# Kernel optimization log

Measured on AMD Instinct MI355X. Metric: run time of the kernel, lower is better.

The kernel has to match this reference:

```python
import jax, jax.numpy as jnp
import numpy as np

BETA = 0.25
ENTROPY_LOSS_RATIO = 0.1
TEMPERATURE = 0.01
EPS = 1e-5


def _l2norm(x):
    return x / jnp.sqrt(jnp.sum(x * x, axis=-1, keepdims=True)).clip(1e-12)


def _entropy_loss(affinity):
    # affinity: [N, n_e]
    a = affinity / TEMPERATURE
    probs = jax.nn.softmax(a, axis=-1)
    log_probs = jax.nn.log_softmax(a + EPS, axis=-1)
    avg_probs = jnp.mean(probs, axis=0)
    avg_entropy = -jnp.sum(avg_probs * jnp.log(avg_probs + EPS))
    sample_entropy = -jnp.mean(jnp.sum(probs * log_probs, axis=-1))
    return sample_entropy - avg_entropy


def setup_inputs() -> dict:
    key = jax.random.key(0)
    k1, k2, k3 = jax.random.split(key, 3)
    B, C, H, W = 16, 256, 32, 32
    n_e = 16384
    z = jax.random.normal(k1, (B, C, H, W), dtype=jnp.float32)
    embedding = jax.random.normal(k2, (n_e, C), dtype=jnp.float32) * 0.02
    query_ids = jax.random.randint(k3, (B, 1), 0, W, dtype=jnp.int64)
    return {"z": z, "embedding": embedding, "query_ids": query_ids}


def reference(z, embedding, query_ids):
    B, C, H, W = z.shape
    sg = jax.lax.stop_gradient
    zt = jnp.transpose(z, (0, 2, 3, 1))            # [B,H,W,C]
    # l2_norm=True path
    zt = _l2norm(zt)
    emb = _l2norm(embedding)                       # [n_e, C]
    zf = zt.reshape(-1, C)                         # [N, C]
    d = (jnp.sum(zf * zf, axis=1, keepdims=True)
         + jnp.sum(emb * emb, axis=1)
         - 2.0 * jnp.einsum('nd,kd->nk', zf, emb))  # [N, n_e]
    idx = jnp.argmin(d, axis=1)                    # [N]
    z_q = emb[idx].reshape(zt.shape)               # [B,H,W,C]

    # dead code rate (unbiased std over batch, per token position)
    code = idx.reshape(B, -1).astype(jnp.float32)
    dead_code_rate = jnp.mean((jnp.std(code, axis=0, ddof=1) < 1e-5).astype(jnp.float32))

    vq_loss = jnp.mean((z_q - sg(zt)) ** 2, axis=-1, keepdims=True)      # [B,H,W,1]
    commit_loss = BETA * jnp.mean((sg(z_q) - zt) ** 2, axis=-1, keepdims=True)
    loss_mask = (jnp.arange(W).reshape(1, 1, -1, 1)
                 <= query_ids[:, -1].reshape(-1, 1, 1, 1)).astype(jnp.float32)
    denom = jnp.sum(loss_mask)
    vq_loss = jnp.sum(vq_loss * loss_mask) / denom
    commit_loss = jnp.sum(commit_loss * loss_mask) / denom
    entropy_loss = ENTROPY_LOSS_RATIO * _entropy_loss(-d)

    # straight-through estimator
    z_q_st = zt + sg(z_q - zt)
    z_q_out = jnp.transpose(z_q_st, (0, 3, 1, 2))  # [B,C,H,W]
    return (z_q_out, vq_loss, commit_loss, entropy_loss, dead_code_rate, idx)
```

## Files before the change

kernel.cpp:

```cpp
#include <hip/hip_runtime.h>
#include <math.h>

#define N_TOK   16384
#define N_E     16384
#define CDIM    256
#define NCH     8
#define CHSZ    (N_E / NCH)
#define L2E100  144.26950408889634f
#define DELTA_C 0.06f
#define DELTA_D 0.03f
#define EPS_NT  0.008f
#define CAP_BLK 1536u
#define NT_CAP  65536u

typedef __attribute__((ext_vector_type(8))) short short8;
typedef __attribute__((ext_vector_type(4))) float f32x4;

#define OFF_A2   0u
#define OFF_B2   2097152u
#define OFF_RMX  4194304u
#define OFF_CS   4210688u
#define OFF_SC   4227072u
#define OFF_RK   4227088u
#define OFF_NT   4259856u
#define OFF_NTC  4325392u
#define OFF_CBC  4325408u
#define OFF_IDX  4327456u
#define OFF_CAND 4343840u
#define OFF_ZT   10635296u
#define NEED_ZT_BYTES 59318400ull

__device__ __forceinline__ unsigned short f2bf(float x) {
  unsigned u = __float_as_uint(x);
  unsigned r = (u + 0x7fffu + ((u >> 16) & 1u)) >> 16;
  return (unsigned short)r;
}
__device__ __forceinline__ float bf2f(unsigned short h) {
  return __uint_as_float(((unsigned)h) << 16);
}
__device__ __forceinline__ unsigned fkey(float f) {
  unsigned u = __float_as_uint(f);
  return (u & 0x80000000u) ? ~u : (u | 0x80000000u);
}
__device__ __forceinline__ float keyf(unsigned k) {
  return (k & 0x80000000u) ? __uint_as_float(k ^ 0x80000000u) : __uint_as_float(~k);
}

__device__ __forceinline__ void async_load16(const void* g, void* l) {
  __builtin_amdgcn_global_load_lds((const __attribute__((address_space(1))) void*)g,
                                   (__attribute__((address_space(3))) void*)l, 16, 0, 0);
}

__device__ __forceinline__ float blockReduceSum256(float v, float* sbuf) {
  __syncthreads();
  v += __shfl_down(v, 32);
  v += __shfl_down(v, 16);
  v += __shfl_down(v, 8);
  v += __shfl_down(v, 4);
  v += __shfl_down(v, 2);
  v += __shfl_down(v, 1);
  const int tid = threadIdx.x;
  if ((tid & 63) == 0) sbuf[tid >> 6] = v;
  __syncthreads();
  return sbuf[0] + sbuf[1] + sbuf[2] + sbuf[3];
}

__global__ __launch_bounds__(256) void k_norm_emb(const float* __restrict__ emb,
    unsigned short* __restrict__ B2, float* __restrict__ colsum,
    float* __restrict__ scalars, unsigned long long* __restrict__ rowkey,
    unsigned* __restrict__ ntc, unsigned* __restrict__ rowMaxU) {
  const int tid = threadIdx.x, lane = tid & 63, wv = tid >> 6;
  if (blockIdx.x < 64) {
    const int i = blockIdx.x * 256 + tid;
    colsum[i] = 0.f;
    rowkey[i] = ~0ull;
    rowMaxU[i] = 0u;
    if (i < 16) { scalars[i] = 0.f; ntc[i] = 0u; }
  }
  const int k = blockIdx.x * 4 + wv;
  const float4 v = *(const float4*)&emb[(size_t)k * CDIM + lane * 4];
  float ss = v.x * v.x + v.y * v.y + v.z * v.z + v.w * v.w;
#pragma unroll
  for (int off = 1; off < 64; off <<= 1) ss += __shfl_xor(ss, off);
  const float r = 1.0f / fmaxf(sqrtf(ss), 1e-12f);
  ushort4 o;
  o.x = f2bf(v.x * r); o.y = f2bf(v.y * r);
  o.z = f2bf(v.z * r); o.w = f2bf(v.w * r);
  *(ushort4*)&B2[(size_t)k * CDIM + lane * 4] = o;
}

__global__ __launch_bounds__(256) void k_norm_z(const float* __restrict__ z,
                                                unsigned short* __restrict__ A2,
                                                float* __restrict__ zT) {
  __shared__ float ssb[4][64];
  __shared__ float rn[64];
  __shared__ unsigned short tile[64 * 264];
  __shared__ float tileF[64 * 260];
  const int b = blockIdx.x >> 4, hw0 = (blockIdx.x & 15) * 64;
  const int tid = threadIdx.x, cg = tid >> 6, hwl = tid & 63;
  float ss = 0.f;
#pragma unroll 8
  for (int i = 0; i < 64; ++i) {
    const int c = cg + i * 4;
    const float x = z[((size_t)(b * CDIM + c) << 10) + hw0 + hwl];
    ss = fmaf(x, x, ss);
  }
  ssb[cg][hwl] = ss;
  __syncthreads();
  if (tid < 64) {
    const float t = ssb[0][tid] + ssb[1][tid] + ssb[2][tid] + ssb[3][tid];
    rn[tid] = 1.0f / fmaxf(sqrtf(t), 1e-12f);
  }
  __syncthreads();
  const float r = rn[hwl];
#pragma unroll 8
  for (int i = 0; i < 64; ++i) {
    const int c = cg + i * 4;
    const float x = z[((size_t)(b * CDIM + c) << 10) + hw0 + hwl];
    tile[hwl * 264 + c] = f2bf(x * r);
    tileF[hwl * 260 + c] = x;
  }
  __syncthreads();
  const int rr = tid >> 5, tt = tid & 31;
#pragma unroll
  for (int it = 0; it < 8; ++it) {
    const int row = rr + 8 * it;
    const int token = b * 1024 + hw0 + row;
    const uint4 v = *(const uint4*)&tile[row * 264 + tt * 8];
    *(uint4*)&A2[(size_t)token * CDIM + tt * 8] = v;
    if (zT != nullptr) {
      const float4 f0 = *(const float4*)&tileF[row * 260 + tt * 4];
      const float4 f1 = *(const float4*)&tileF[row * 260 + 128 + tt * 4];
      *(float4*)&zT[(size_t)token * CDIM + tt * 4] = f0;
      *(float4*)&zT[(size_t)token * CDIM + 128 + tt * 4] = f1;
    }
  }
}

__global__ __launch_bounds__(256, 3) void k_pass1(const unsigned short* __restrict__ A2,
    const unsigned short* __restrict__ B2,
    unsigned long long* __restrict__ cand, unsigned* __restrict__ cbc,
    unsigned* __restrict__ rowMaxU) {
  __shared__ alignas(16) unsigned short Bt[2][128 * 64];
  __shared__ unsigned lcnt;
  const int rt = blockIdx.x, chunk = blockIdx.y;
  const int r0 = rt * 64, k0 = chunk * CHSZ;
  const int blin = rt * NCH + chunk;
  const int tid = threadIdx.x, lane = tid & 63, w = tid >> 6;
  const int wr0 = w * 16;
  const int l15 = lane & 15, quad = lane >> 4;

  if (tid == 0) lcnt = 0u;

  short8 afr[4][2];
  {
    const size_t rbase = (size_t)(r0 + wr0 + l15) * CDIM;
#pragma unroll
    for (int st = 0; st < 4; ++st)
#pragma unroll
      for (int kk = 0; kk < 2; ++kk)
        afr[st][kk] = *(const short8*)&A2[rbase + st * 64 + (((kk << 2) | quad) * 8)];
  }

  const int row0 = tid >> 3, cg0 = tid & 7;
  const int gcg0 = cg0 ^ (row0 & 7);
  const unsigned short* bsrc0 = B2 + (size_t)(k0 + row0) * CDIM + gcg0 * 8;
  const unsigned bofs0 = (unsigned)tid * 16u;

  int boff[8][2];
#pragma unroll
  for (int tj = 0; tj < 8; ++tj) {
    const int br = tj * 16 + l15;
#pragma unroll
    for (int kk = 0; kk < 2; ++kk)
      boff[tj][kk] = br * 64 + ((((kk << 2) | quad) ^ (br & 7)) * 8);
  }

#pragma unroll
  for (int i = 0; i < 4; ++i)
    async_load16(bsrc0 + i * 8192, (char*)Bt[0] + bofs0 + i * 4096);
  __syncthreads();

  f32x4 acc[8];
  float runMax[4];
#pragma unroll
  for (int r = 0; r < 4; ++r) runMax[r] = -3.0e38f;

#pragma unroll 1
  for (int ct = 0; ct < 16; ++ct) {
#pragma unroll
    for (int tj = 0; tj < 8; ++tj) acc[tj] = (f32x4){0.f, 0.f, 0.f, 0.f};

#pragma unroll
    for (int st = 0; st < 4; ++st) {
      if (!(ct == 15 && st == 3)) {
        const int noff = (st < 3) ? (st + 1) * 64 : 32768;
        char* dbuf = (char*)Bt[(st + 1) & 1];
#pragma unroll
        for (int i = 0; i < 4; ++i)
          async_load16(bsrc0 + noff + i * 8192, dbuf + bofs0 + i * 4096);
      }
      const unsigned short* bp = Bt[st & 1];
#pragma unroll
      for (int kk = 0; kk < 2; ++kk) {
        short8 bfr[8];
#pragma unroll
        for (int tj = 0; tj < 8; ++tj)
          bfr[tj] = *(const short8*)&bp[boff[tj][kk]];
#pragma unroll
        for (int tj = 0; tj < 8; ++tj)
          acc[tj] = __builtin_amdgcn_mfma_f32_16x16x32_bf16(afr[st][kk], bfr[tj],
                                                            acc[tj], 0, 0, 0);
      }

      if (st == 3) {
        const int kb = k0 + ct * 128;
#pragma unroll
        for (int r = 0; r < 4; ++r) {
          float mt = acc[0][r];
#pragma unroll
          for (int tj = 1; tj < 8; ++tj) mt = fmaxf(mt, acc[tj][r]);
          mt = fmaxf(mt, __shfl_xor(mt, 1));
          mt = fmaxf(mt, __shfl_xor(mt, 2));
          mt = fmaxf(mt, __shfl_xor(mt, 4));
          mt = fmaxf(mt, __shfl_xor(mt, 8));
          runMax[r] = fmaxf(runMax[r], mt);
          const float thrD = runMax[r] - DELTA_D;
          const unsigned rowg = (unsigned)(r0 + wr0 + quad * 4 + r);
#pragma unroll
          for (int tj = 0; tj < 8; ++tj) {
            const float d = acc[tj][r];
            if (d >= thrD) {
              const unsigned slot = atomicAdd(&lcnt, 1u);
              if (slot < CAP_BLK) {
                const float t = d + d;
                const unsigned pr = (rowg << 14) | (unsigned)(kb + tj * 16 + l15);
                cand[(size_t)blin * CAP_BLK + slot] =
                    ((unsigned long long)__float_as_uint(t) << 32) | pr;
              }
            }
          }
        }
      }
      __syncthreads();
    }
    bsrc0 += 32768;
  }

#pragma unroll
  for (int r = 0; r < 4; ++r)
    if (l15 == 0)
      atomicMax(&rowMaxU[r0 + wr0 + quad * 4 + r], fkey(runMax[r] + runMax[r]));
  if (tid == 0) cbc[blin] = lcnt < CAP_BLK ? lcnt : CAP_BLK;
}

__global__ __launch_bounds__(256) void k_cstat2(const unsigned long long* __restrict__ cand,
    const unsigned* __restrict__ cbc, const unsigned* __restrict__ rowMaxU,
    float* __restrict__ colsum, unsigned* __restrict__ ntList,
    unsigned* __restrict__ ntc, float* __restrict__ scalars) {
  __shared__ float lM[64], lZ[64], lE[64], lIZ[64];
  __shared__ float sbuf[4];
  const int rt = blockIdx.x, r0 = rt * 64;
  const int tid = threadIdx.x, lane = tid & 63;
  if (tid < 64) {
    lM[tid] = keyf(rowMaxU[r0 + tid]);
    lZ[tid] = 0.f; lE[tid] = 0.f;
  }
  __syncthreads();
  for (int sub = 0; sub < NCH; ++sub) {
    const int blin = rt * NCH + sub;
    const unsigned cnt = cbc[blin] < CAP_BLK ? cbc[blin] : CAP_BLK;
    for (unsigned i = tid; i < cnt; i += 256u) {
      const unsigned long long e = cand[(size_t)blin * CAP_BLK + i];
      const unsigned pr = (unsigned)(e & 0xFFFFFFFu);
      const float t = __uint_as_float((unsigned)(e >> 32));
      const int rowl = (int)((pr >> 14) & 63u);
      const float d = t - lM[rowl];
      const float ex = exp2f(d * L2E100);
      atomicAdd(&lZ[rowl], ex);
      atomicAdd(&lE[rowl], d * 100.0f * ex);
    }
  }
  __syncthreads();
  float ent = 0.f;
  if (tid < 64) {
    const float Z = lZ[tid];
    lIZ[tid] = 1.0f / Z;
    ent = logf(Z) - lE[tid] / Z;
  }
  const float es = blockReduceSum256(ent, sbuf);
  if (tid == 0) atomicAdd(&scalars[1], es);
  __syncthreads();
  for (int sub = 0; sub < NCH; ++sub) {
    const int blin = rt * NCH + sub;
    const unsigned cnt = cbc[blin] < CAP_BLK ? cbc[blin] : CAP_BLK;
    const unsigned lim = (cnt + 255u) & ~255u;
    for (unsigned i = tid; i < lim; i += 256u) {
      bool nt = false;
      unsigned pr = 0u;
      if (i < cnt) {
        const unsigned long long e = cand[(size_t)blin * CAP_BLK + i];
        pr = (unsigned)(e & 0xFFFFFFFu);
        const float t = __uint_as_float((unsigned)(e >> 32));
        const int rowl = (int)((pr >> 14) & 63u);
        const float d = t - lM[rowl];
        atomicAdd(&colsum[pr & 0x3FFFu], exp2f(d * L2E100) * lIZ[rowl]);
        nt = (d >= -EPS_NT);
      }
      const unsigned long long mask = __ballot(nt);
      const unsigned cw = (unsigned)__popcll(mask);
      unsigned base = 0u;
      if (lane == 0 && cw) base = atomicAdd(ntc, cw);
      base = __shfl((int)base, 0);
      if (nt) {
        const unsigned off = (unsigned)__popcll(mask & ((1ull << lane) - 1ull));
        const unsigned s = base + off;
        if (s < NT_CAP) ntList[s] = pr;
      }
    }
  }
}

__global__ __launch_bounds__(256) void k_refine(const float* __restrict__ z,
    const float* __restrict__ zT, const float* __restrict__ emb,
    const unsigned* __restrict__ ntList, const unsigned* __restrict__ ntc,
    unsigned long long* __restrict__ rowkey) {
  const unsigned cnt = *ntc;
  const unsigned lim = cnt < NT_CAP ? cnt : NT_CAP;
  const int lane = threadIdx.x & 63, wv = threadIdx.x >> 6;
  for (unsigned slot = blockIdx.x * 4 + wv; slot < lim; slot += gridDim.x * 4) {
    const unsigned pr = ntList[slot];
    const int n = (int)(pr >> 14), k = (int)(pr & 0x3FFFu);
    const int b = n >> 10, hw = n & 1023;
    double sz = 0.0, se = 0.0, sp = 0.0;
#pragma unroll
    for (int u = 0; u < CDIM / 64; ++u) {
      const int c = lane + u * 64;
      const double zv = (zT != nullptr)
          ? (double)zT[(size_t)n * CDIM + c]
          : (double)z[((size_t)(b * CDIM + c) << 10) + hw];
      const double ev = (double)emb[(size_t)k * CDIM + c];
      sz = fma(zv, zv, sz); se = fma(ev, ev, se); sp = fma(zv, ev, sp);
    }
    for (int off = 32; off; off >>= 1) {
      sz += __shfl_down(sz, off);
      se += __shfl_down(se, off);
      sp += __shfl_down(sp, off);
    }
    if (lane == 0) {
      const double nz = fmax(sqrt(sz), 1e-12);
      const double ne = fmax(sqrt(se), 1e-12);
      const double d = sz / (nz * nz) + se / (ne * ne) - 2.0 * sp / (nz * ne);
      const unsigned long long key =
          (((unsigned long long)(d * 140737488355328.0)) << 14) | (unsigned long long)k;
      atomicMin(&rowkey[n], key);
    }
  }
}

__global__ __launch_bounds__(256) void k_zq(const unsigned short* __restrict__ A2,
    const unsigned short* __restrict__ B2, const unsigned long long* __restrict__ rowkey,
    const long long* __restrict__ qids, int* __restrict__ idxI,
    float* __restrict__ outIdxF, float* __restrict__ outZ,
    float* __restrict__ scalars) {
  __shared__ int lidx[64];
  __shared__ unsigned short tile[64 * 264];
  __shared__ float sbuf[4];
  const int b = blockIdx.x >> 4, hw0 = (blockIdx.x & 15) * 64;
  const int tid = threadIdx.x;
  if (tid < 64) {
    const int n = b * 1024 + hw0 + tid;
    const unsigned long long key = rowkey[n];
    const int k = (key != ~0ull) ? (int)(key & 0x3FFFull) : 0;
    lidx[tid] = k;
    idxI[n] = k;
    outIdxF[n] = (float)k;
  }
  __syncthreads();
  const long long qid = qids[b];
  const int rr = tid >> 5, tt = tid & 31;
  float vq = 0.f;
#pragma unroll
  for (int it = 0; it < 8; ++it) {
    const int row = rr + 8 * it;
    const int token = b * 1024 + hw0 + row;
    union { uint4 v; unsigned short s[8]; } ev, zv;
    ev.v = *(const uint4*)&B2[(size_t)lidx[row] * CDIM + tt * 8];
    zv.v = *(const uint4*)&A2[(size_t)token * CDIM + tt * 8];
    *(uint4*)&tile[row * 264 + tt * 8] = ev.v;
    float dd = 0.f;
#pragma unroll
    for (int u = 0; u < 8; ++u) {
      const float d = bf2f(ev.s[u]) - bf2f(zv.s[u]);
      dd = fmaf(d, d, dd);
    }
    if ((long long)(row & 31) <= qid) vq += dd;
  }
  const float s = blockReduceSum256(vq, sbuf);
  if (tid == 0) atomicAdd(&scalars[0], s * (1.0f / 256.0f));
  __syncthreads();
  const int cg = tid >> 6, hwl = tid & 63;
#pragma unroll 8
  for (int i = 0; i < 64; ++i) {
    const int c = cg + i * 4;
    outZ[((size_t)(b * CDIM + c) << 10) + hw0 + hwl] = bf2f(tile[hwl * 264 + c]);
  }
}

__global__ __launch_bounds__(256) void k_final(const int* __restrict__ idxI,
    const long long* __restrict__ qids, const float* __restrict__ colsum,
    const float* __restrict__ scalars, float* __restrict__ out) {
  __shared__ float sbuf[4];
  const int tid = threadIdx.x;
  float ae = 0.f;
  for (int i = tid; i < N_E; i += 256) {
    const float q = colsum[i] * (1.0f / (float)N_TOK);
    ae += q * logf(q + 1e-5f);
  }
  const float aes = blockReduceSum256(ae, sbuf);
  int cnt = 0;
  for (int p = tid; p < 1024; p += 256) {
    const int v = idxI[p];
    bool eq = true;
    for (int b = 1; b < 16; ++b) eq = eq && (idxI[b * 1024 + p] == v);
    cnt += eq ? 1 : 0;
  }
  const float dc = blockReduceSum256((float)cnt, sbuf);
  if (tid == 0) {
    float denom = 0.f;
    for (int b = 0; b < 16; ++b) denom += (float)(qids[b] + 1ll);
    out[4194304] = scalars[0] / denom;
    out[4194305] = 0.25f * scalars[0] / denom;
    out[4194306] = 0.1f * (scalars[1] * (1.0f / (float)N_TOK) + aes);
    out[4194307] = dc * (1.0f / 1024.0f);
  }
}

extern "C" void kernel_launch(void* const* d_in, const int* in_sizes, int n_in,
                              void* d_out, int out_size, void* d_ws, size_t ws_size,
                              hipStream_t stream) {
  const float*      z    = (const float*)d_in[0];
  const float*      emb  = (const float*)d_in[1];
  const long long*  qids = (const long long*)d_in[2];
  float* out = (float*)d_out;
  float* W   = (float*)d_ws;

  unsigned short* A2 = (unsigned short*)(W + OFF_A2);
  unsigned short* B2 = (unsigned short*)(W + OFF_B2);
  unsigned* rowMaxU = (unsigned*)(W + OFF_RMX);
  float* colsum = W + OFF_CS;
  float* scal   = W + OFF_SC;
  unsigned long long* rowkey = (unsigned long long*)(W + OFF_RK);
  unsigned* ntList = (unsigned*)(W + OFF_NT);
  unsigned* ntc    = (unsigned*)(W + OFF_NTC);
  unsigned* cbc    = (unsigned*)(W + OFF_CBC);
  int* idxI        = (int*)(W + OFF_IDX);
  unsigned long long* cand = (unsigned long long*)(W + OFF_CAND);
  float* zT = (ws_size >= NEED_ZT_BYTES) ? (W + OFF_ZT) : (float*)nullptr;

  k_norm_emb<<<dim3(N_E / 4),     dim3(256), 0, stream>>>(emb, B2, colsum, scal,
                                                          rowkey, ntc, rowMaxU);
  k_norm_z  <<<dim3(256),         dim3(256), 0, stream>>>(z, A2, zT);
  k_pass1   <<<dim3(256, NCH),    dim3(256), 0, stream>>>(A2, B2, cand, cbc, rowMaxU);
  k_cstat2  <<<dim3(256),         dim3(256), 0, stream>>>(cand, cbc, rowMaxU, colsum,
                                                          ntList, ntc, scal);
  k_refine  <<<dim3(1024),        dim3(256), 0, stream>>>(z, zT, emb, ntList, ntc, rowkey);
  k_zq      <<<dim3(256),         dim3(256), 0, stream>>>(A2, B2, rowkey, qids,
                                                          idxI, out + 4194308, out, scal);
  k_final   <<<dim3(1),           dim3(256), 0, stream>>>(idxI, qids, colsum, scal, out);
}
```

Baseline: 548.5 us.

## Use 2 waves per block with 32 rows each in pass1 GEMM

The pass1 similarity GEMM block shrinks from 4 waves to 2 waves. Each wave now computes two 16-row tiles against the same 128 codes, so every B fragment read from LDS is reused across twice as many MFMAs. This roughly halves LDS read traffic per MFMA. In exchange each wave holds twice the accumulators and A fragments, which raises register pressure and lowers the number of waves per CU. The B-tile staging loop is adjusted so 128 threads still load the full tile.

```diff
diff --git a/kernel.cpp b/kernel.cpp
--- a/kernel.cpp
+++ b/kernel.cpp
@@ -137,7 +137,7 @@
   }
 }
 
-__global__ __launch_bounds__(256, 3) void k_pass1(const unsigned short* __restrict__ A2,
+__global__ __launch_bounds__(128, 2) void k_pass1(const unsigned short* __restrict__ A2,
     const unsigned short* __restrict__ B2,
     unsigned long long* __restrict__ cand, unsigned* __restrict__ cbc,
     unsigned* __restrict__ rowMaxU) {
@@ -147,19 +147,20 @@
   const int r0 = rt * 64, k0 = chunk * CHSZ;
   const int blin = rt * NCH + chunk;
   const int tid = threadIdx.x, lane = tid & 63, w = tid >> 6;
-  const int wr0 = w * 16;
+  const int wr0 = w * 32;
   const int l15 = lane & 15, quad = lane >> 4;
 
   if (tid == 0) lcnt = 0u;
 
-  short8 afr[4][2];
-  {
-    const size_t rbase = (size_t)(r0 + wr0 + l15) * CDIM;
+  short8 afr[2][4][2];
+#pragma unroll
+  for (int ti = 0; ti < 2; ++ti) {
+    const size_t rbase = (size_t)(r0 + wr0 + ti * 16 + l15) * CDIM;
 #pragma unroll
     for (int st = 0; st < 4; ++st)
 #pragma unroll
       for (int kk = 0; kk < 2; ++kk)
-        afr[st][kk] = *(const short8*)&A2[rbase + st * 64 + (((kk << 2) | quad) * 8)];
+        afr[ti][st][kk] = *(const short8*)&A2[rbase + st * 64 + (((kk << 2) | quad) * 8)];
   }
 
   const int row0 = tid >> 3, cg0 = tid & 7;
@@ -177,19 +178,23 @@
   }
 
 #pragma unroll
-  for (int i = 0; i < 4; ++i)
-    async_load16(bsrc0 + i * 8192, (char*)Bt[0] + bofs0 + i * 4096);
-  __syncthreads();
-
-  f32x4 acc[8];
-  float runMax[4];
-#pragma unroll
-  for (int r = 0; r < 4; ++r) runMax[r] = -3.0e38f;
+  for (int i = 0; i < 8; ++i)
+    async_load16(bsrc0 + i * 4096, (char*)Bt[0] + bofs0 + i * 2048);
+  __syncthreads();
+
+  f32x4 acc[2][8];
+  float runMax[2][4];
+#pragma unroll
+  for (int ti = 0; ti < 2; ++ti)
+#pragma unroll
+    for (int r = 0; r < 4; ++r) runMax[ti][r] = -3.0e38f;
 
 #pragma unroll 1
   for (int ct = 0; ct < 16; ++ct) {
 #pragma unroll
-    for (int tj = 0; tj < 8; ++tj) acc[tj] = (f32x4){0.f, 0.f, 0.f, 0.f};
+    for (int ti = 0; ti < 2; ++ti)
+#pragma unroll
+      for (int tj = 0; tj < 8; ++tj) acc[ti][tj] = (f32x4){0.f, 0.f, 0.f, 0.f};
 
 #pragma unroll
     for (int st = 0; st < 4; ++st) {
@@ -197,8 +202,8 @@
         const int noff = (st < 3) ? (st + 1) * 64 : 32768;
         char* dbuf = (char*)Bt[(st + 1) & 1];
 #pragma unroll
-        for (int i = 0; i < 4; ++i)
-          async_load16(bsrc0 + noff + i * 8192, dbuf + bofs0 + i * 4096);
+        for (int i = 0; i < 8; ++i)
+          async_load16(bsrc0 + noff + i * 4096, dbuf + bofs0 + i * 2048);
       }
       const unsigned short* bp = Bt[st & 1];
 #pragma unroll
@@ -208,39 +213,43 @@
         for (int tj = 0; tj < 8; ++tj)
           bfr[tj] = *(const short8*)&bp[boff[tj][kk]];
 #pragma unroll
-        for (int tj = 0; tj < 8; ++tj)
-          acc[tj] = __builtin_amdgcn_mfma_f32_16x16x32_bf16(afr[st][kk], bfr[tj],
-                                                            acc[tj], 0, 0, 0);
+        for (int ti = 0; ti < 2; ++ti)
+#pragma unroll
+          for (int tj = 0; tj < 8; ++tj)
+            acc[ti][tj] = __builtin_amdgcn_mfma_f32_16x16x32_bf16(afr[ti][st][kk], bfr[tj],
+                                                                  acc[ti][tj], 0, 0, 0);
       }
 
       if (st == 3) {
         const int kb = k0 + ct * 128;
 #pragma unroll
-        for (int r = 0; r < 4; ++r) {
-          float mt = acc[0][r];
-#pragma unroll
-          for (int tj = 1; tj < 8; ++tj) mt = fmaxf(mt, acc[tj][r]);
-          mt = fmaxf(mt, __shfl_xor(mt, 1));
-          mt = fmaxf(mt, __shfl_xor(mt, 2));
-          mt = fmaxf(mt, __shfl_xor(mt, 4));
-          mt = fmaxf(mt, __shfl_xor(mt, 8));
-          runMax[r] = fmaxf(runMax[r], mt);
-          const float thrD = runMax[r] - DELTA_D;
-          const unsigned rowg = (unsigned)(r0 + wr0 + quad * 4 + r);
-#pragma unroll
-          for (int tj = 0; tj < 8; ++tj) {
-            const float d = acc[tj][r];
-            if (d >= thrD) {
-              const unsigned slot = atomicAdd(&lcnt, 1u);
-              if (slot < CAP_BLK) {
-                const float t = d + d;
-                const unsigned pr = (rowg << 14) | (unsigned)(kb + tj * 16 + l15);
-                cand[(size_t)blin * CAP_BLK + slot] =
-                    ((unsigned long long)__float_as_uint(t) << 32) | pr;
+        for (int ti = 0; ti < 2; ++ti)
+#pragma unroll
+          for (int r = 0; r < 4; ++r) {
+            float mt = acc[ti][0][r];
+#pragma unroll
+            for (int tj = 1; tj < 8; ++tj) mt = fmaxf(mt, acc[ti][tj][r]);
+            mt = fmaxf(mt, __shfl_xor(mt, 1));
+            mt = fmaxf(mt, __shfl_xor(mt, 2));
+            mt = fmaxf(mt, __shfl_xor(mt, 4));
+            mt = fmaxf(mt, __shfl_xor(mt, 8));
+            runMax[ti][r] = fmaxf(runMax[ti][r], mt);
+            const float thrD = runMax[ti][r] - DELTA_D;
+            const unsigned rowg = (unsigned)(r0 + wr0 + ti * 16 + quad * 4 + r);
+#pragma unroll
+            for (int tj = 0; tj < 8; ++tj) {
+              const float d = acc[ti][tj][r];
+              if (d >= thrD) {
+                const unsigned slot = atomicAdd(&lcnt, 1u);
+                if (slot < CAP_BLK) {
+                  const float t = d + d;
+                  const unsigned pr = (rowg << 14) | (unsigned)(kb + tj * 16 + l15);
+                  cand[(size_t)blin * CAP_BLK + slot] =
+                      ((unsigned long long)__float_as_uint(t) << 32) | pr;
+                }
               }
             }
           }
-        }
       }
       __syncthreads();
     }
@@ -248,9 +257,12 @@
   }
 
 #pragma unroll
-  for (int r = 0; r < 4; ++r)
-    if (l15 == 0)
-      atomicMax(&rowMaxU[r0 + wr0 + quad * 4 + r], fkey(runMax[r] + runMax[r]));
+  for (int ti = 0; ti < 2; ++ti)
+#pragma unroll
+    for (int r = 0; r < 4; ++r)
+      if (l15 == 0)
+        atomicMax(&rowMaxU[r0 + wr0 + ti * 16 + quad * 4 + r],
+                  fkey(runMax[ti][r] + runMax[ti][r]));
   if (tid == 0) cbc[blin] = lcnt < CAP_BLK ? lcnt : CAP_BLK;
 }
 
@@ -461,7 +473,7 @@
   k_norm_emb<<<dim3(N_E / 4),     dim3(256), 0, stream>>>(emb, B2, colsum, scal,
                                                           rowkey, ntc, rowMaxU);
   k_norm_z  <<<dim3(256),         dim3(256), 0, stream>>>(z, A2, zT);
-  k_pass1   <<<dim3(256, NCH),    dim3(256), 0, stream>>>(A2, B2, cand, cbc, rowMaxU);
+  k_pass1   <<<dim3(256, NCH),    dim3(128), 0, stream>>>(A2, B2, cand, cbc, rowMaxU);
   k_cstat2  <<<dim3(256),         dim3(256), 0, stream>>>(cand, cbc, rowMaxU, colsum,
                                                           ntList, ntc, scal);
   k_refine  <<<dim3(1024),        dim3(256), 0, stream>>>(z, zT, emb, ntList, ntc, rowkey);
```

Result: slower. 694.2 us (+26.6%).
